# Kernel optimization log

Hardware: AMD Instinct MI355X
Metric: run time of the kernel (lower is better)

The kernel has to match this reference:

```python
import jax, jax.numpy as jnp
import numpy as np

D, H = 256, 4            # model dim, num heads
HD = D // H              # head dim (even, needed by rotate_half)
B, N, M, NS = 2, 6, 512, 512  # batch, views, t keypoints, s keypoints
EPS = 1e-5


def _linear(x, w, b):
    return x @ w + b


def _ln(x, g, b):
    mu = x.mean(-1, keepdims=True)
    var = ((x - mu) ** 2).mean(-1, keepdims=True)
    return (x - mu) * jax.lax.rsqrt(var + EPS) * g + b


def _ffn(x, f1w, f1b, lng, lnb, f2w, f2b):
    # Linear(2d,2d) -> LayerNorm -> exact GELU -> Linear(2d,d)
    h = jax.nn.gelu(_ln(_linear(x, f1w, f1b), lng, lnb), approximate=False)
    return _linear(h, f2w, f2b)


def _rotate_half(x):
    # pairs (x0,x1) -> (-x1, x0), interleaved
    return jnp.stack((-x[..., 1::2], x[..., 0::2]), axis=-1).reshape(x.shape)


def _rope(freqs, t):
    return t * freqs[0] + _rotate_half(t) * freqs[1]


def _attn(q, k, v):
    sim = jnp.einsum('...id,...jd->...ij', q, k) * (q.shape[-1] ** -0.5)
    return jnp.einsum('...ij,...jd->...id', jax.nn.softmax(sim, axis=-1), v)


def _self_block(x, enc, qkv_w, qkv_b, out_w, out_b, *ffn_p):
    b, n_img, m, d = x.shape
    enc = jnp.swapaxes(enc, 2, 3)  # encoding.dim()==6 path
    qkv = _linear(x, qkv_w, qkv_b).reshape(b, n_img, m, H, HD, 3)
    qkv = jnp.swapaxes(qkv, -4, -3)  # [b,N,H,m,hd,3]
    q, k, v = qkv[..., 0], qkv[..., 1], qkv[..., 2]
    ctx = _attn(_rope(enc, q), _rope(enc, k), v)  # [b,N,H,m,hd]
    msg = _linear(jnp.swapaxes(ctx, -3, -2).reshape(b, n_img, m, d), out_w, out_b)
    return x + _ffn(jnp.concatenate([x, msg], -1), *ffn_p)


def _t2t_block(t, qkv_w, qkv_b, out_w, out_b, *ffn_p):
    t2 = jnp.swapaxes(t, 1, 2)  # [b,m,N,d]
    b, m, n_img, d = t2.shape
    qkv = _linear(t2, qkv_w, qkv_b).reshape(b, m, n_img, H, HD, 3)
    qkv = jnp.swapaxes(qkv, 3, 2)  # [b,m,H,N,hd,3]
    q, k, v = qkv[..., 0], qkv[..., 1], qkv[..., 2]
    ctx = _attn(q, k, v)  # [b,m,H,N,hd]
    msg = _linear(jnp.swapaxes(ctx, 3, 2).reshape(b, m, n_img, d), out_w, out_b)
    return jnp.swapaxes(t2 + _ffn(jnp.concatenate([t2, msg], -1), *ffn_p), 1, 2)


def _s2s_block(s, q_enc, k_enc, qkv_w, qkv_b, out_w, out_b, *ffn_p):
    b, n_img, n, d = s.shape
    qkv = _linear(s, qkv_w, qkv_b).reshape(b, n_img, n, H, HD, 3)
    qkv = jnp.swapaxes(jnp.swapaxes(qkv, -4, -3), -5, -4)  # [b,H,N,n,hd,3]
    q, k, v = qkv[..., 0], qkv[..., 1], qkv[..., 2]
    # expand queries across all views, RoPE per (i,j) view pair
    q = jnp.broadcast_to(q[:, :, None], (b, H, n_img, n_img, n, HD))
    q = _rope(q_enc, q).reshape(b, H, n_img, n_img * n, HD)
    k = _rope(k_enc, k)
    ctx = _attn(q, k, v).reshape(b, H, n_img, n_img, n, HD)
    # drop diagonal (i==j) entries exactly like boolean-mask indexing in torch
    off = np.nonzero(~np.eye(n_img, dtype=bool).ravel())[0]
    ctx = ctx.reshape(b, H, n_img * n_img, n, HD)[:, :, off]
    ctx = ctx.reshape(b, H, n_img - 1, n_img, n, HD).mean(2)  # [b,H,N,n,hd]
    ctx = jnp.swapaxes(jnp.swapaxes(ctx, 1, 2), 2, 3).reshape(b, n_img, n, d)
    msg = _linear(ctx, out_w, out_b)
    return s + _ffn(jnp.concatenate([s, msg], -1), *ffn_p)


def _cross_block(d0, d1, q_w, q_b, kv_w, kv_b, out_w, out_b, *ffn_p):
    b, n_img, m, d = d0.shape
    m1 = d1.shape[2]
    q = jnp.swapaxes(_linear(d0, q_w, q_b).reshape(b, n_img, m, H, HD), 2, 3)
    kv = jnp.swapaxes(_linear(d1, kv_w, kv_b).reshape(b, n_img, m1, H, HD, 2), 2, 3)
    ctx = _attn(q, kv[..., 0], kv[..., 1])  # [b,N,H,m,hd]
    msg = _linear(jnp.swapaxes(ctx, 2, 3).reshape(b, n_img, m, d), out_w, out_b)
    return d0 + _ffn(jnp.concatenate([d0, msg], -1), *ffn_p)


def setup_inputs() -> dict:
    key = jax.random.key(0)
    ks = iter(jax.random.split(key, 80))
    f32 = jnp.float32

    def lin(din, dout):
        return (jax.random.normal(next(ks), (din, dout), f32) * (din ** -0.5),
                jnp.zeros((dout,), f32))

    inp = {}
    inp['t_desc'] = jax.random.normal(next(ks), (B, N, M, D), f32)
    inp['s_desc'] = jax.random.normal(next(ks), (B, N, NS, D), f32)
    inp['t_encoding'] = jax.random.normal(next(ks), (2, 1, 1, N, M, HD), f32)
    inp['s_encoding'] = jax.random.normal(next(ks), (2, 1, 1, N, NS, HD), f32)
    inp['q_encoding'] = jax.random.normal(next(ks), (2, 1, 1, N, N, 1, HD), f32)
    inp['k_encoding'] = jax.random.normal(next(ks), (2, 1, 1, N, NS, HD), f32)
    for pre in ('sa', 'ss', 'tt'):
        inp[pre + '_qkv_w'], inp[pre + '_qkv_b'] = lin(D, 3 * D)
        inp[pre + '_out_w'], inp[pre + '_out_b'] = lin(D, D)
        inp[pre + '_f1_w'], inp[pre + '_f1_b'] = lin(2 * D, 2 * D)
        inp[pre + '_ln_g'] = jnp.ones((2 * D,), f32)
        inp[pre + '_ln_b'] = jnp.zeros((2 * D,), f32)
        inp[pre + '_f2_w'], inp[pre + '_f2_b'] = lin(2 * D, D)
    inp['ca_q_w'], inp['ca_q_b'] = lin(D, D)
    inp['ca_kv_w'], inp['ca_kv_b'] = lin(D, 2 * D)
    inp['ca_out_w'], inp['ca_out_b'] = lin(D, D)
    inp['ca_f1_w'], inp['ca_f1_b'] = lin(2 * D, 2 * D)
    inp['ca_ln_g'] = jnp.ones((2 * D,), f32)
    inp['ca_ln_b'] = jnp.zeros((2 * D,), f32)
    inp['ca_f2_w'], inp['ca_f2_b'] = lin(2 * D, D)
    inp['cf_w1'], inp['cf_b1'] = lin(D, D)
    inp['cf_w2'], inp['cf_b2'] = lin(D, 1)
    return inp


def reference(t_desc, s_desc, t_encoding, s_encoding, q_encoding, k_encoding,
              sa_qkv_w, sa_qkv_b, sa_out_w, sa_out_b, sa_f1_w, sa_f1_b, sa_ln_g, sa_ln_b, sa_f2_w, sa_f2_b,
              ss_qkv_w, ss_qkv_b, ss_out_w, ss_out_b, ss_f1_w, ss_f1_b, ss_ln_g, ss_ln_b, ss_f2_w, ss_f2_b,
              tt_qkv_w, tt_qkv_b, tt_out_w, tt_out_b, tt_f1_w, tt_f1_b, tt_ln_g, tt_ln_b, tt_f2_w, tt_f2_b,
              ca_q_w, ca_q_b, ca_kv_w, ca_kv_b, ca_out_w, ca_out_b, ca_f1_w, ca_f1_b, ca_ln_g, ca_ln_b, ca_f2_w, ca_f2_b,
              cf_w1, cf_b1, cf_w2, cf_b2):
    sa = (sa_qkv_w, sa_qkv_b, sa_out_w, sa_out_b, sa_f1_w, sa_f1_b, sa_ln_g, sa_ln_b, sa_f2_w, sa_f2_b)
    t = _self_block(t_desc, t_encoding, *sa)   # shared SelfBlock weights
    s = _self_block(s_desc, s_encoding, *sa)
    t = _t2t_block(t, tt_qkv_w, tt_qkv_b, tt_out_w, tt_out_b, tt_f1_w, tt_f1_b, tt_ln_g, tt_ln_b, tt_f2_w, tt_f2_b)
    s = _s2s_block(s, q_encoding, k_encoding, ss_qkv_w, ss_qkv_b, ss_out_w, ss_out_b, ss_f1_w, ss_f1_b, ss_ln_g, ss_ln_b, ss_f2_w, ss_f2_b)
    ca = (ca_q_w, ca_q_b, ca_kv_w, ca_kv_b, ca_out_w, ca_out_b, ca_f1_w, ca_f1_b, ca_ln_g, ca_ln_b, ca_f2_w, ca_f2_b)
    t2 = _cross_block(t, s, *ca)               # shared CrossBlock weights
    s2 = _cross_block(s, t, *ca)
    conf = _linear(jax.nn.relu(_linear(jax.lax.stop_gradient(s), cf_w1, cf_b1)), cf_w2, cf_b2)[..., 0]
    return t2, s2, conf
```

## Files before the change

### kernel.cpp

```cpp
#include <hip/hip_runtime.h>
#include <hip/hip_bf16.h>
#include <math.h>

constexpr int kD   = 256;
constexpr int kH   = 4;
constexpr int kHD  = 64;
constexpr int kB   = 2;
constexpr int kN   = 6;
constexpr int kM   = 512;
constexpr int kRowsH = kB*kN*kM;
constexpr int kRows  = 2*kRowsH;
constexpr int kGrpH  = kB*kN*kH;
constexpr int kGrp   = 2*kGrpH;
constexpr size_t kTOK = (size_t)kRowsH*kD;
constexpr size_t kEncSlab = (size_t)kN*kM*kHD;
constexpr size_t kQEncSlab = (size_t)kN*kN*kHD;
constexpr float kL2E = 1.4426950408889634f;

typedef unsigned short u16;
typedef __attribute__((ext_vector_type(8))) short s16x8;
typedef __attribute__((ext_vector_type(4))) float f32x4;

__device__ __forceinline__ float wred_sum(float v){
  #pragma unroll
  for (int m=32;m>0;m>>=1) v += __shfl_xor(v, m, 64);
  return v;
}
__device__ __forceinline__ u16 f2b(float x){
  union { float f; unsigned u; } a; a.f = x;
  unsigned r = a.u + 0x7fffu + ((a.u >> 16) & 1u);
  return (u16)(r >> 16);
}
__device__ __forceinline__ float b2f(u16 x){
  union { unsigned u; float f; } a; a.u = ((unsigned)x) << 16;
  return a.f;
}
__device__ __forceinline__ unsigned pk2(float lo, float hi){
  union { __hip_bfloat162 h2; unsigned u; } c;
  c.h2 = __float22bfloat162_rn(make_float2(lo, hi));
  return c.u;
}

struct FuseArgs {
  const float* Wout[4]; const float* W1[4];
  const float* bout[4]; const float* b1[4];
  float* Wtmp; float* b1p;
};

__global__ __launch_bounds__(256) void wfuse_k(FuseArgs fa)
{
  const int set = blockIdx.x >> 5;
  const int t = blockIdx.x & 31;
  const int row0 = (t >> 3)*64, col0 = (t & 7)*64;
  const float* A  = fa.Wout[set];
  const float* Bm = fa.W1[set] + 256*512;
  float* C = fa.Wtmp + (size_t)set*(256*512);
  __shared__ float As[16][65];
  __shared__ float Bs[16][64];
  const int tid = threadIdx.x;
  const int tx = tid & 15, ty = tid >> 4;
  const int ar = tid >> 2, ak = (tid & 3)*4;
  const int wr = tid >> 4, wc = (tid & 15)*4;
  float acc[4][4] = {};
  for (int kt = 0; kt < 256; kt += 16) {
    float4 av = *(const float4*)(A + (size_t)(row0+ar)*256 + kt + ak);
    As[ak+0][ar]=av.x; As[ak+1][ar]=av.y; As[ak+2][ar]=av.z; As[ak+3][ar]=av.w;
    *(float4*)(&Bs[wr][wc]) = *(const float4*)(Bm + (size_t)(kt+wr)*512 + col0 + wc);
    __syncthreads();
    #pragma unroll
    for (int k2=0;k2<16;++k2) {
      float a[4], b[4];
      #pragma unroll
      for (int i=0;i<4;++i) a[i]=As[k2][ty*4+i];
      #pragma unroll
      for (int j=0;j<4;++j) b[j]=Bs[k2][tx*4+j];
      #pragma unroll
      for (int i=0;i<4;++i)
        #pragma unroll
        for (int j=0;j<4;++j) acc[i][j] = fmaf(a[i], b[j], acc[i][j]);
    }
    __syncthreads();
  }
  #pragma unroll
  for (int i=0;i<4;++i)
    #pragma unroll
    for (int j=0;j<4;++j)
      C[(size_t)(row0+ty*4+i)*512 + col0+tx*4+j] = acc[i][j];
}

__global__ __launch_bounds__(256) void biasfuse_k(FuseArgs fa)
{
  const int set = blockIdx.x >> 1;
  const int n = (blockIdx.x & 1)*256 + threadIdx.x;
  const float* W1 = fa.W1[set];
  const float* bo = fa.bout[set];
  float s = fa.b1[set][n];
  for (int k = 0; k < 256; ++k)
    s = fmaf(bo[k], W1[(size_t)(256+k)*512 + n], s);
  fa.b1p[set*512 + n] = s;
}

struct WtDesc { const float* W; const float* W2; u16* Wt; int K; int N; int ntiles; };
struct WtTable { WtDesc d[18]; };

__global__ __launch_bounds__(256) void wtcast_k(WtTable tab)
{
  int t = blockIdx.x, mi = 0;
  while (t >= tab.d[mi].ntiles) { t -= tab.d[mi].ntiles; ++mi; }
  const float* W = tab.d[mi].W;
  const float* W2 = tab.d[mi].W2;
  u16* Wt = tab.d[mi].Wt;
  const int K = tab.d[mi].K, N = tab.d[mi].N;
  const int ktn = K >> 5;
  const int nt = t / ktn, kt = t % ktn;
  const int n0 = nt*128, k0 = kt*32;
  u16* dst = Wt + (size_t)t*4096;
  #pragma unroll
  for (int s = 0; s < 2; ++s) {
    const int idx0 = (s*256 + (int)threadIdx.x)*8;
    const int ar = idx0 >> 5;
    const int w8 = (idx0 >> 3) & 3;
    const int sw = (ar >> 1) & 3;
    int kk = k0 + ((w8 ^ sw) << 3);
    const int n  = n0 + ar;
    const float* src = W;
    if (W2 && kk >= 256) { src = W2; kk -= 256; }
    union { u16 u[8]; s16x8 v; } o;
    #pragma unroll
    for (int e = 0; e < 8; ++e)
      o.u[e] = f2b(src[(size_t)(kk + e)*N + n]);
    *(s16x8*)(dst + idx0) = o.v;
  }
}

template<bool A1B, bool A2B, bool CB>
__global__ __launch_bounds__(256) void mmad_k(
    const void* __restrict__ A1a, const void* __restrict__ A1b,
    const void* __restrict__ A2a, const void* __restrict__ A2b, int K1,
    const u16* __restrict__ Wa, const u16* __restrict__ Wb,
    const float* __restrict__ bia, const float* __restrict__ bib,
    const float* __restrict__ bi2a, const float* __restrict__ bi2b, int Ns,
    const float* __restrict__ Ra, const float* __restrict__ Rb,
    void* __restrict__ Cp, int N, int K, int Mh, int doRelu)
{
  __shared__ u16 As[2][128*32];
  __shared__ u16 Bs[2][128*32];
  const int tid = threadIdx.x;
  const int lane = tid & 63, w = tid >> 6;
  const int gx = gridDim.x;
  const int nblk = gx * gridDim.y;
  int flat = blockIdx.y*gx + blockIdx.x;
  if (!(nblk & 7)) flat = (flat & 7)*(nblk >> 3) + (flat >> 3);
  const int bxx = flat % gx, byy = flat / gx;
  const int row0 = byy*128, col0 = bxx*128;
  const bool sec = (row0 >= Mh);
  const int lr0 = sec ? row0 - Mh : row0;
  const void* A1 = sec ? A1b : A1a;
  const void* A2 = sec ? A2b : A2a;
  const u16* Wt  = sec ? Wb : Wa;
  const float* bias  = sec ? bib : bia;
  const float* bias2 = sec ? bi2b : bi2a;
  const float* R = sec ? Rb : Ra;
  const int wr = (w >> 1)*64, wc = (w & 1)*64;
  const int ar = tid >> 1, ah = tid & 1;
  const int K2 = K - K1;
  const int ktn = K >> 5;
  f32x4 acc[4][4] = {};

  auto stage = [&](int buf, int kt) {
    const u16* wtile = Wt + ((size_t)((col0 >> 7)*ktn + (kt >> 5)))*4096;
    #pragma unroll
    for (int s = 0; s < 2; ++s) {
      const u16* srcp = wtile + (size_t)(s*256 + tid)*8;
      __builtin_amdgcn_global_load_lds(
          (const __attribute__((address_space(1))) void*)srcp,
          (__attribute__((address_space(3))) void*)((char*)Bs[buf] + s*4096 + w*1024),
          16, 0, 0);
    }
    const int kk = kt + ah*16;
    union { u16 u[16]; s16x8 v[2]; } tmp;
    if (kk < K1) {
      if constexpr (A1B) {
        const u16* ap = (const u16*)A1 + (size_t)(lr0+ar)*K1 + kk;
        tmp.v[0] = *(const s16x8*)ap; tmp.v[1] = *(const s16x8*)(ap+8);
      } else {
        const float* ap = (const float*)A1 + (size_t)(lr0+ar)*K1 + kk;
        #pragma unroll
        for (int i = 0; i < 16; i += 4) {
          f32x4 v4 = *(const f32x4*)(ap + i);
          tmp.u[i+0]=f2b(v4.x); tmp.u[i+1]=f2b(v4.y); tmp.u[i+2]=f2b(v4.z); tmp.u[i+3]=f2b(v4.w);
        }
      }
    } else {
      if constexpr (A2B) {
        const u16* ap = (const u16*)A2 + (size_t)(lr0+ar)*K2 + (kk - K1);
        tmp.v[0] = *(const s16x8*)ap; tmp.v[1] = *(const s16x8*)(ap+8);
      } else {
        const float* ap = (const float*)A2 + (size_t)(lr0+ar)*K2 + (kk - K1);
        #pragma unroll
        for (int i = 0; i < 16; i += 4) {
          f32x4 v4 = *(const f32x4*)(ap + i);
          tmp.u[i+0]=f2b(v4.x); tmp.u[i+1]=f2b(v4.y); tmp.u[i+2]=f2b(v4.z); tmp.u[i+3]=f2b(v4.w);
        }
      }
    }
    const int sw = (ar >> 1) & 3;
    *(s16x8*)(&As[buf][ar*32 + ((ah*2+0)^sw)*8]) = tmp.v[0];
    *(s16x8*)(&As[buf][ar*32 + ((ah*2+1)^sw)*8]) = tmp.v[1];
  };

  stage(0, 0);
  __syncthreads();
  for (int t = 0; t < ktn; ++t) {
    const int cur = t & 1;
    if (t + 1 < ktn) stage(cur ^ 1, (t + 1) << 5);
    s16x8 af[4], bfv[4];
    #pragma unroll
    for (int fm = 0; fm < 4; ++fm) {
      const int r = wr + fm*16 + (lane & 15);
      const int g = (lane >> 4) ^ ((r >> 1) & 3);
      af[fm] = *(const s16x8*)(&As[cur][r*32 + g*8]);
    }
    #pragma unroll
    for (int fn = 0; fn < 4; ++fn) {
      const int c = wc + fn*16 + (lane & 15);
      const int g = (lane >> 4) ^ ((c >> 1) & 3);
      bfv[fn] = *(const s16x8*)(&Bs[cur][c*32 + g*8]);
    }
    #pragma unroll
    for (int fm = 0; fm < 4; ++fm)
      #pragma unroll
      for (int fn = 0; fn < 4; ++fn)
        acc[fm][fn] = __builtin_amdgcn_mfma_f32_16x16x32_bf16(af[fm], bfv[fn], acc[fm][fn], 0, 0, 0);
    __syncthreads();
  }

  #pragma unroll
  for (int fm = 0; fm < 4; ++fm) {
    const int ro = wr + fm*16 + (lane >> 4)*4;
    #pragma unroll
    for (int fn = 0; fn < 4; ++fn) {
      const int cc = col0 + wc + fn*16 + (lane & 15);
      const float bv = (cc < Ns) ? bias[cc] : bias2[cc - Ns];
      #pragma unroll
      for (int j = 0; j < 4; ++j) {
        float v = acc[fm][fn][j] + bv;
        if (R) v += R[(size_t)(lr0 + ro + j)*N + cc];
        if (doRelu) v = fmaxf(v, 0.f);
        const size_t idx = (size_t)(row0 + ro + j)*N + cc;
        if constexpr (CB) ((u16*)Cp)[idx] = f2b(v);
        else              ((float*)Cp)[idx] = v;
      }
    }
  }
}

__global__ __launch_bounds__(256) void prep_self_k(
    const u16* __restrict__ qkvU, const float* __restrict__ t_enc,
    const float* __restrict__ s_enc,
    u16* __restrict__ Qb, u16* __restrict__ Kb, u16* __restrict__ Vt)
{
  __shared__ u16 vs[64][66];
  const int g = blockIdx.x >> 3, i0 = (blockIdx.x & 7)*64;
  const int h = g & 3, bn = g >> 2;
  const float* enc = (bn < 12) ? t_enc : s_enc;
  const int n = (bn < 12 ? bn : bn - 12) % kN;
  const int c = threadIdx.x & 63, t4 = threadIdx.x >> 6;
  const float sgn = (c & 1) ? 1.f : -1.f;
  #pragma unroll 4
  for (int rr = 0; rr < 16; ++rr) {
    const int il = rr*4 + t4, i = i0 + il;
    const u16* base = qkvU + ((size_t)bn*kM + i)*768 + h*192;
    const float q = b2f(base[c*3]), k = b2f(base[c*3+1]);
    const float qp = b2f(base[(c^1)*3]), kp = b2f(base[(c^1)*3+1]);
    const size_t eo = ((size_t)(n*kM + i))*kHD + c;
    const float e0 = enc[eo], e1 = enc[kEncSlab + eo];
    Qb[((size_t)g*kM + i)*kHD + c] = f2b((q*e0 + sgn*qp*e1)*0.125f);
    Kb[((size_t)g*kM + i)*kHD + c] = f2b(k*e0 + sgn*kp*e1);
    vs[il][c] = base[c*3+2];
  }
  __syncthreads();
  #pragma unroll 4
  for (int rr = 0; rr < 16; ++rr) {
    const int cc = rr*4 + t4;
    Vt[((size_t)g*kHD + cc)*kM + i0 + c] = vs[c][cc];
  }
}

__global__ __launch_bounds__(256) void prep_s2s_k(
    const u16* __restrict__ qkvU, const float* __restrict__ kenc,
    float* __restrict__ Qs, u16* __restrict__ Kb, u16* __restrict__ Vt)
{
  __shared__ u16 vs[64][66];
  const int g = blockIdx.x >> 3, i0 = (blockIdx.x & 7)*64;
  const int view = g % kN, bh = g / kN;
  const int h = bh & 3, b = bh >> 2;
  const int c = threadIdx.x & 63, t4 = threadIdx.x >> 6;
  const float sgn = (c & 1) ? 1.f : -1.f;
  #pragma unroll 4
  for (int rr = 0; rr < 16; ++rr) {
    const int il = rr*4 + t4, i = i0 + il;
    const u16* base = qkvU + ((size_t)(kRowsH + (b*kN+view)*kM + i))*768 + h*192;
    const float k = b2f(base[c*3+1]), kp = b2f(base[(c^1)*3+1]);
    const size_t eo = ((size_t)(view*kM + i))*kHD + c;
    const float e0 = kenc[eo], e1 = kenc[kEncSlab + eo];
    Qs[((size_t)g*kM + i)*kHD + c] = b2f(base[c*3]);
    Kb[((size_t)g*kM + i)*kHD + c] = f2b(k*e0 + sgn*kp*e1);
    vs[il][c] = base[c*3+2];
  }
  __syncthreads();
  #pragma unroll 4
  for (int rr = 0; rr < 16; ++rr) {
    const int cc = rr*4 + t4;
    Vt[((size_t)g*kHD + cc)*kM + i0 + c] = vs[c][cc];
  }
}

__global__ __launch_bounds__(256) void prep_cross_k(
    const u16* __restrict__ qkvC, u16* __restrict__ Kb, u16* __restrict__ Vt)
{
  __shared__ u16 vs[64][66];
  const int g = blockIdx.x >> 3, i0 = (blockIdx.x & 7)*64;
  const int h = g & 3, bn = g >> 2;
  const int src = (bn < 12) ? bn + 12 : bn - 12;
  const int c = threadIdx.x & 63, t4 = threadIdx.x >> 6;
  #pragma unroll 4
  for (int rr = 0; rr < 16; ++rr) {
    const int il = rr*4 + t4, i = i0 + il;
    const u16* base = qkvC + ((size_t)src*kM + i)*768 + 256 + h*128;
    Kb[((size_t)g*kM + i)*kHD + c] = f2b(b2f(base[c*2]) * 0.125f);
    vs[il][c] = base[c*2+1];
  }
  __syncthreads();
  #pragma unroll 4
  for (int rr = 0; rr < 16; ++rr) {
    const int cc = rr*4 + t4;
    Vt[((size_t)g*kHD + cc)*kM + i0 + c] = vs[c][cc];
  }
}

template<int CROSSQ>
__global__ __launch_bounds__(256) void attn_mm_k(
    const u16* __restrict__ Qb, const u16* __restrict__ Kb,
    const u16* __restrict__ Vt, u16* __restrict__ ctx)
{
  const int w = threadIdx.x >> 6, lane = threadIdx.x & 63;
  const int bij = (blockIdx.x & 7)*48 + (blockIdx.x >> 3);
  const int g = bij >> 2, qblk = bij & 3;
  const int h = g & 3, bn = g >> 2;
  const int q0 = qblk*128 + w*32;
  const int qr = lane & 15, hi = lane >> 4;
  const bool subhi = (hi & 1), up = (hi >= 2);

  s16x8 qf0[2], qf1[2];
  #pragma unroll
  for (int f = 0; f < 2; ++f) {
    const u16* qp = CROSSQ
      ? Qb + ((size_t)(bn*kM + q0 + f*16 + qr))*768 + h*kHD + hi*8
      : Qb + ((size_t)g*kM + q0 + f*16 + qr)*kHD + hi*8;
    qf0[f] = *(const s16x8*)(qp);
    qf1[f] = *(const s16x8*)(qp + 32);
  }

  const u16* Kg = Kb + (size_t)g*kM*kHD;
  const u16* Vg = Vt + (size_t)g*kHD*kM;
  f32x4 acc[2][4] = {};
  float m[2] = {-1e30f, -1e30f}, l[2] = {0.f, 0.f};

  for (int kc = 0; kc < 16; ++kc) {
    const int k0 = kc*32;
    s16x8 a0[2], a1[2];
    #pragma unroll
    for (int t = 0; t < 2; ++t) {
      const u16* kp = Kg + ((size_t)(k0 + t*16 + qr))*kHD + hi*8;
      a0[t] = *(const s16x8*)(kp);
      a1[t] = *(const s16x8*)(kp + 32);
    }
    s16x8 pa[2];
    #pragma unroll
    for (int f = 0; f < 2; ++f) {
      f32x4 st[2];
      #pragma unroll
      for (int t = 0; t < 2; ++t) {
        f32x4 z = {0.f, 0.f, 0.f, 0.f};
        z = __builtin_amdgcn_mfma_f32_16x16x32_bf16(a0[t], qf0[f], z, 0, 0, 0);
        z = __builtin_amdgcn_mfma_f32_16x16x32_bf16(a1[t], qf1[f], z, 0, 0, 0);
        st[t] = z;
      }
      float mloc = fmaxf(fmaxf(fmaxf(st[0][0], st[0][1]), fmaxf(st[0][2], st[0][3])),
                         fmaxf(fmaxf(st[1][0], st[1][1]), fmaxf(st[1][2], st[1][3])));
      mloc = fmaxf(mloc, __shfl_xor(mloc, 16));
      mloc = fmaxf(mloc, __shfl_xor(mloc, 32));
      if (!__all(mloc - m[f] <= 8.f)) {
        const float mn = fmaxf(m[f], mloc);
        const float r = exp2f((m[f] - mn)*kL2E);
        m[f] = mn;
        l[f] *= r;
        const float rr0 = __shfl(r, hi*4+0), rr1 = __shfl(r, hi*4+1);
        const float rr2 = __shfl(r, hi*4+2), rr3 = __shfl(r, hi*4+3);
        #pragma unroll
        for (int db = 0; db < 4; ++db) {
          acc[f][db][0] *= rr0; acc[f][db][1] *= rr1;
          acc[f][db][2] *= rr2; acc[f][db][3] *= rr3;
        }
      }
      float p[8], ls = 0.f;
      #pragma unroll
      for (int t = 0; t < 2; ++t)
        #pragma unroll
        for (int j = 0; j < 4; ++j) {
          const float pv = exp2f((st[t][j] - m[f])*kL2E);
          p[t*4+j] = pv; ls += pv;
        }
      l[f] += ls;
      const unsigned c00 = pk2(p[0], p[1]);
      const unsigned c01 = pk2(p[2], p[3]);
      const unsigned c10 = pk2(p[4], p[5]);
      const unsigned c11 = pk2(p[6], p[7]);
      const unsigned c00x = __shfl_xor((int)c00, 32), c10x = __shfl_xor((int)c10, 32);
      const unsigned c01x = __shfl_xor((int)c01, 32), c11x = __shfl_xor((int)c11, 32);
      const unsigned E = up ? c10x : c00, F = up ? c10 : c00x;
      const unsigned G = up ? c11x : c01, H = up ? c11 : c01x;
      const unsigned Ex = __shfl_xor((int)E, 16), Fx = __shfl_xor((int)F, 16);
      const unsigned Gx = __shfl_xor((int)G, 16), Hx = __shfl_xor((int)H, 16);
      union { unsigned w[4]; s16x8 v; } pw;
      pw.w[0] = subhi ? Fx : E;
      pw.w[1] = subhi ? Hx : G;
      pw.w[2] = subhi ? F  : Ex;
      pw.w[3] = subhi ? H  : Gx;
      pa[f] = pw.v;
    }
    #pragma unroll
    for (int db = 0; db < 4; ++db) {
      const u16* vp = Vg + ((size_t)(db*16 + qr))*kM + k0 + hi*8;
      const s16x8 vf = *(const s16x8*)(vp);
      acc[0][db] = __builtin_amdgcn_mfma_f32_16x16x32_bf16(pa[0], vf, acc[0][db], 0, 0, 0);
      acc[1][db] = __builtin_amdgcn_mfma_f32_16x16x32_bf16(pa[1], vf, acc[1][db], 0, 0, 0);
    }
  }

  #pragma unroll
  for (int f = 0; f < 2; ++f) {
    float lf = l[f];
    lf += __shfl_xor(lf, 16); lf += __shfl_xor(lf, 32);
    const float li = 1.f/lf;
    const float l0 = __shfl(li, hi*4+0), l1 = __shfl(li, hi*4+1);
    const float l2 = __shfl(li, hi*4+2), l3 = __shfl(li, hi*4+3);
    #pragma unroll
    for (int db = 0; db < 4; ++db) {
      const size_t base = ((size_t)(bn*kM + q0 + f*16 + hi*4))*kD + h*kHD + db*16 + qr;
      ctx[base + 0*kD] = f2b(acc[f][db][0]*l0);
      ctx[base + 1*kD] = f2b(acc[f][db][1]*l1);
      ctx[base + 2*kD] = f2b(acc[f][db][2]*l2);
      ctx[base + 3*kD] = f2b(acc[f][db][3]*l3);
    }
  }
}

__device__ __forceinline__ void rope4(const f32x4 x, const f32x4 e0, const f32x4 e1, float o[4])
{
  o[0] = x[0]*e0[0] - x[1]*e1[0];
  o[1] = x[1]*e0[1] + x[0]*e1[1];
  o[2] = x[2]*e0[2] - x[3]*e1[2];
  o[3] = x[3]*e0[3] + x[2]*e1[3];
}

__global__ __launch_bounds__(256) void attn_s2s_k(
    const float* __restrict__ Qraw, const u16* __restrict__ Kb,
    const u16* __restrict__ Vt, const float* __restrict__ qenc,
    u16* __restrict__ ctx5)
{
  const int w = threadIdx.x >> 6, lane = threadIdx.x & 63;
  const int bij = (blockIdx.x & 7)*120 + (blockIdx.x >> 3);
  const int bh = bij / 120;
  const int rest = bij % 120;
  const int col = rest / 20;
  const int rem = rest % 20;
  const int qblk = rem / 5, split = rem % 5;
  const int q0 = qblk*128 + w*32;
  const int qr = lane & 15, hi = lane >> 4;
  const bool subhi = (hi & 1), up = (hi >= 2);

  const int e  = split*6 + col;
  const int iv = e/5;
  const int j0 = e%5;
  const int jv = j0 + (j0 >= iv ? 1 : 0);

  s16x8 qf0[2], qf1[2];
  #pragma unroll
  for (int f = 0; f < 2; ++f) {
    const float* qp = Qraw + ((size_t)(bh*kN + jv)*kM + q0 + f*16 + qr)*kHD + hi*8;
    const float* ep = qenc + ((size_t)(iv*kN + jv))*kHD + hi*8;
    union { u16 u[8]; s16x8 v; } A, B;
    float o[4];
    rope4(*(const f32x4*)(qp),   *(const f32x4*)(ep),   *(const f32x4*)(ep+kQEncSlab), o);
    #pragma unroll
    for (int j = 0; j < 4; ++j) A.u[j] = f2b(o[j]*0.125f);
    rope4(*(const f32x4*)(qp+4), *(const f32x4*)(ep+4), *(const f32x4*)(ep+kQEncSlab+4), o);
    #pragma unroll
    for (int j = 0; j < 4; ++j) A.u[4+j] = f2b(o[j]*0.125f);
    rope4(*(const f32x4*)(qp+32), *(const f32x4*)(ep+32), *(const f32x4*)(ep+kQEncSlab+32), o);
    #pragma unroll
    for (int j = 0; j < 4; ++j) B.u[j] = f2b(o[j]*0.125f);
    rope4(*(const f32x4*)(qp+36), *(const f32x4*)(ep+36), *(const f32x4*)(ep+kQEncSlab+36), o);
    #pragma unroll
    for (int j = 0; j < 4; ++j) B.u[4+j] = f2b(o[j]*0.125f);
    qf0[f] = A.v; qf1[f] = B.v;
  }

  const int g2 = bh*kN + iv;
  const u16* Kg = Kb + (size_t)g2*kM*kHD;
  const u16* Vg = Vt + (size_t)g2*kHD*kM;
  f32x4 acc[2][4] = {};
  float m[2] = {-1e30f, -1e30f}, l[2] = {0.f, 0.f};

  for (int kc = 0; kc < 16; ++kc) {
    const int k0 = kc*32;
    s16x8 a0[2], a1[2];
    #pragma unroll
    for (int t = 0; t < 2; ++t) {
      const u16* kp = Kg + ((size_t)(k0 + t*16 + qr))*kHD + hi*8;
      a0[t] = *(const s16x8*)(kp);
      a1[t] = *(const s16x8*)(kp + 32);
    }
    s16x8 pa[2];
    #pragma unroll
    for (int f = 0; f < 2; ++f) {
      f32x4 st[2];
      #pragma unroll
      for (int t = 0; t < 2; ++t) {
        f32x4 z = {0.f, 0.f, 0.f, 0.f};
        z = __builtin_amdgcn_mfma_f32_16x16x32_bf16(a0[t], qf0[f], z, 0, 0, 0);
        z = __builtin_amdgcn_mfma_f32_16x16x32_bf16(a1[t], qf1[f], z, 0, 0, 0);
        st[t] = z;
      }
      float mloc = fmaxf(fmaxf(fmaxf(st[0][0], st[0][1]), fmaxf(st[0][2], st[0][3])),
                         fmaxf(fmaxf(st[1][0], st[1][1]), fmaxf(st[1][2], st[1][3])));
      mloc = fmaxf(mloc, __shfl_xor(mloc, 16));
      mloc = fmaxf(mloc, __shfl_xor(mloc, 32));
      if (!__all(mloc - m[f] <= 8.f)) {
        const float mn = fmaxf(m[f], mloc);
        const float r = exp2f((m[f] - mn)*kL2E);
        m[f] = mn;
        l[f] *= r;
        const float rr0 = __shfl(r, hi*4+0), rr1 = __shfl(r, hi*4+1);
        const float rr2 = __shfl(r, hi*4+2), rr3 = __shfl(r, hi*4+3);
        #pragma unroll
        for (int db = 0; db < 4; ++db) {
          acc[f][db][0] *= rr0; acc[f][db][1] *= rr1;
          acc[f][db][2] *= rr2; acc[f][db][3] *= rr3;
        }
      }
      float p[8], ls = 0.f;
      #pragma unroll
      for (int t = 0; t < 2; ++t)
        #pragma unroll
        for (int j = 0; j < 4; ++j) {
          const float pv = exp2f((st[t][j] - m[f])*kL2E);
          p[t*4+j] = pv; ls += pv;
        }
      l[f] += ls;
      const unsigned c00 = pk2(p[0], p[1]);
      const unsigned c01 = pk2(p[2], p[3]);
      const unsigned c10 = pk2(p[4], p[5]);
      const unsigned c11 = pk2(p[6], p[7]);
      const unsigned c00x = __shfl_xor((int)c00, 32), c10x = __shfl_xor((int)c10, 32);
      const unsigned c01x = __shfl_xor((int)c01, 32), c11x = __shfl_xor((int)c11, 32);
      const unsigned E = up ? c10x : c00, F = up ? c10 : c00x;
      const unsigned G = up ? c11x : c01, H = up ? c11 : c01x;
      const unsigned Ex = __shfl_xor((int)E, 16), Fx = __shfl_xor((int)F, 16);
      const unsigned Gx = __shfl_xor((int)G, 16), Hx = __shfl_xor((int)H, 16);
      union { unsigned w[4]; s16x8 v; } pw;
      pw.w[0] = subhi ? Fx : E;
      pw.w[1] = subhi ? Hx : G;
      pw.w[2] = subhi ? F  : Ex;
      pw.w[3] = subhi ? H  : Gx;
      pa[f] = pw.v;
    }
    #pragma unroll
    for (int db = 0; db < 4; ++db) {
      const u16* vp = Vg + ((size_t)(db*16 + qr))*kM + k0 + hi*8;
      const s16x8 vf = *(const s16x8*)(vp);
      acc[0][db] = __builtin_amdgcn_mfma_f32_16x16x32_bf16(pa[0], vf, acc[0][db], 0, 0, 0);
      acc[1][db] = __builtin_amdgcn_mfma_f32_16x16x32_bf16(pa[1], vf, acc[1][db], 0, 0, 0);
    }
  }

  const int b = bh >> 2, h = bh & 3;
  u16* outp = ctx5 + (size_t)split*kTOK;
  #pragma unroll
  for (int f = 0; f < 2; ++f) {
    float lf = l[f];
    lf += __shfl_xor(lf, 16); lf += __shfl_xor(lf, 32);
    const float li = 0.2f/lf;
    const float l0 = __shfl(li, hi*4+0), l1 = __shfl(li, hi*4+1);
    const float l2 = __shfl(li, hi*4+2), l3 = __shfl(li, hi*4+3);
    #pragma unroll
    for (int db = 0; db < 4; ++db) {
      const size_t base = ((size_t)((b*kN + col)*kM + q0 + f*16 + hi*4))*kD + h*kHD + db*16 + qr;
      outp[base + 0*kD] = f2b(acc[f][db][0]*l0);
      outp[base + 1*kD] = f2b(acc[f][db][1]*l1);
      outp[base + 2*kD] = f2b(acc[f][db][2]*l2);
      outp[base + 3*kD] = f2b(acc[f][db][3]*l3);
    }
  }
}

__global__ __launch_bounds__(256) void sum5_k(const u16* __restrict__ c5,
                                              u16* __restrict__ outU)
{
  const size_t i4 = ((size_t)blockIdx.x*256 + threadIdx.x)*4;
  float s0=0.f, s1=0.f, s2=0.f, s3=0.f;
  #pragma unroll
  for (int sp = 0; sp < 5; ++sp) {
    uint2 d = *(const uint2*)(c5 + sp*kTOK + i4);
    s0 += b2f((u16)(d.x & 0xffff)); s1 += b2f((u16)(d.x >> 16));
    s2 += b2f((u16)(d.y & 0xffff)); s3 += b2f((u16)(d.y >> 16));
  }
  union { u16 u[4]; uint2 d; } o;
  o.u[0]=f2b(s0); o.u[1]=f2b(s1); o.u[2]=f2b(s2); o.u[3]=f2b(s3);
  *(uint2*)(outU + i4) = o.d;
}

__global__ __launch_bounds__(256) void attn_t2t_k(
    const u16* __restrict__ qkvU, u16* __restrict__ ctxU)
{
  const int wid = blockIdx.x*4 + (threadIdx.x >> 6);
  const int lane = threadIdx.x & 63;
  const int m = wid & 511;
  const int t = wid >> 9;
  const int nq = t % kN;
  const int bh = t / kN;
  const int h = bh & 3, b = bh >> 2;
  const u16* pb[kN];
  #pragma unroll
  for (int nk = 0; nk < kN; ++nk)
    pb[nk] = qkvU + ((size_t)(b*kN+nk)*kM + m)*768 + h*192;
  const float qc = b2f(pb[nq][lane*3]);
  float sim[kN];
  #pragma unroll
  for (int nk = 0; nk < kN; ++nk)
    sim[nk] = wred_sum(qc * b2f(pb[nk][lane*3+1])) * 0.125f;
  float mx = sim[0];
  #pragma unroll
  for (int nk = 1; nk < kN; ++nk) mx = fmaxf(mx, sim[nk]);
  float p[kN], s = 0.f;
  #pragma unroll
  for (int nk = 0; nk < kN; ++nk) { p[nk] = expf(sim[nk]-mx); s += p[nk]; }
  const float inv = 1.f/s;
  float o = 0.f;
  #pragma unroll
  for (int nk = 0; nk < kN; ++nk) o = fmaf(p[nk], b2f(pb[nk][lane*3+2]), o);
  ctxU[((size_t)(b*kN+nq)*kM + m)*kD + h*kHD + lane] = f2b(o*inv);
}

__global__ __launch_bounds__(256) void lngelu_k(
    const float* __restrict__ x, u16* __restrict__ y,
    const float* __restrict__ g0, const float* __restrict__ b0,
    const float* __restrict__ g1, const float* __restrict__ b1, int Mh)
{
  const int row = blockIdx.x;
  const int tid = threadIdx.x;
  const float* g = (row < Mh) ? g0 : g1;
  const float* bb = (row < Mh) ? b0 : b1;
  const float* xr = x + (size_t)row*512;
  const float v0 = xr[tid], v1 = xr[tid+256];
  const int w = tid >> 6, lane = tid & 63;
  __shared__ float red[2][4];
  const float s1 = wred_sum(v0+v1);
  const float s2 = wred_sum(v0*v0+v1*v1);
  if (lane == 0){ red[0][w]=s1; red[1][w]=s2; }
  __syncthreads();
  const float mean = (red[0][0]+red[0][1]+red[0][2]+red[0][3]) * (1.f/512.f);
  const float ms   = (red[1][0]+red[1][1]+red[1][2]+red[1][3]) * (1.f/512.f);
  const float rs = rsqrtf(ms - mean*mean + 1e-5f);
  const float y0 = (v0-mean)*rs*g[tid]     + bb[tid];
  const float y1 = (v1-mean)*rs*g[tid+256] + bb[tid+256];
  y[(size_t)row*512 + tid]     = f2b(0.5f*y0*(1.f+erff(y0*0.70710678118654752f)));
  y[(size_t)row*512 + tid+256] = f2b(0.5f*y1*(1.f+erff(y1*0.70710678118654752f)));
}

__global__ void conf_dot_k(const float* __restrict__ tmp, const float* __restrict__ w2,
                           const float* __restrict__ b2, float* __restrict__ out)
{
  const int w = threadIdx.x >> 6, lane = threadIdx.x & 63;
  const int row = blockIdx.x*4 + w;
  const float* t = tmp + (size_t)row*kD;
  float s = 0.f;
  #pragma unroll
  for (int j=0;j<4;++j) s = fmaf(t[lane+j*64], w2[lane+j*64], s);
  s = wred_sum(s);
  if (lane == 0) out[row] = s + b2[0];
}

extern "C" void kernel_launch(void* const* d_in, const int* in_sizes, int n_in,
                              void* d_out, int out_size, void* d_ws, size_t ws_size,
                              hipStream_t stream)
{
  auto F = [&](int i){ return (const float*)d_in[i]; };
  const float* t_desc = F(0);
  const float* s_desc = F(1);
  const float* t_enc  = F(2);
  const float* s_enc  = F(3);
  const float* q_enc  = F(4);
  const float* k_enc  = F(5);

  char* base = (char*)d_ws;
  float* xts = (float*)base;
  float* xt = xts;
  float* xs = xts + kTOK;
  char* R1  = base + 2*kTOK*sizeof(float);
  char* CTX = R1 + 4*kTOK*sizeof(float);
  char* MSG = CTX + 2*kTOK*sizeof(u16);
  u16* Qb16 = (u16*)(MSG + kTOK*sizeof(float));
  u16* Kb16 = Qb16 + 2*kTOK;
  u16* Vt16 = Kb16 + 2*kTOK;
  u16* wsW  = Vt16 + 2*kTOK;
  u16*   qkvU  = (u16*)R1;
  float* hbuf  = (float*)R1;
  u16*   ctx5  = (u16*)R1;
  float* Wtmp  = (float*)R1;
  u16*   ctxU  = (u16*)CTX;
  float* Qs2s  = (float*)MSG;
  float* confb = (float*)MSG;
  u16*   yU    = (u16*)CTX;

  float* out_t2s2 = (float*)d_out;
  float* out_conf = (float*)d_out + 2*kTOK;

  WtTable tab;
  int nd = 0, total_tiles = 0;
  size_t woff = 0;
  const u16* wp[18];
  auto addw = [&](int idx, const float* W2, int K, int N){
    u16* dst = wsW + woff;
    tab.d[nd] = { F(idx), W2, dst, K, N, (N>>7)*(K>>5) };
    total_tiles += tab.d[nd].ntiles;
    wp[nd] = dst;
    woff += (size_t)K*N;
    ++nd;
    return nd-1;
  };
  const int W_SA_QKV = addw(6,  nullptr, 256, 768);
  const int W_SA_F1  = addw(10, Wtmp + 0*131072, 512, 512);
  const int W_SA_F2  = addw(14, nullptr, 512, 256);
  const int W_SS_QKV = addw(16, nullptr, 256, 768);
  const int W_SS_F1  = addw(20, Wtmp + 1*131072, 512, 512);
  const int W_SS_F2  = addw(24, nullptr, 512, 256);
  const int W_TT_QKV = addw(26, nullptr, 256, 768);
  const int W_TT_F1  = addw(30, Wtmp + 2*131072, 512, 512);
  const int W_TT_F2  = addw(34, nullptr, 512, 256);
  const int W_CA_Q   = addw(36, nullptr, 256, 256);
  const int W_CA_KV  = addw(38, nullptr, 256, 512);
  const int W_CA_F1  = addw(42, Wtmp + 3*131072, 512, 512);
  const int W_CA_F2  = addw(46, nullptr, 512, 256);
  const int W_CF_1   = addw(48, nullptr, 256, 256);
  (void)W_CA_KV;
  float* b1p = (float*)(wsW + woff);

  FuseArgs fa;
  fa.Wout[0]=F(8);  fa.Wout[1]=F(18); fa.Wout[2]=F(28); fa.Wout[3]=F(40);
  fa.W1[0]=F(10);   fa.W1[1]=F(20);   fa.W1[2]=F(30);   fa.W1[3]=F(42);
  fa.bout[0]=F(9);  fa.bout[1]=F(19); fa.bout[2]=F(29); fa.bout[3]=F(41);
  fa.b1[0]=F(11);   fa.b1[1]=F(21);   fa.b1[2]=F(31);   fa.b1[3]=F(43);
  fa.Wtmp = Wtmp; fa.b1p = b1p;
  wfuse_k<<<128, 256, 0, stream>>>(fa);
  biasfuse_k<<<8, 256, 0, stream>>>(fa);
  wtcast_k<<<total_tiles, 256, 0, stream>>>(tab);

  auto mm_f32_to_b16 = [&](const float* a1a, const float* a1b, int wa, int wb2,
                           const float* ba, const float* bb2, u16* c, int N_, int K_){
    dim3 grid(N_/128, kRows/128);
    mmad_k<false,false,true><<<grid,256,0,stream>>>(a1a, a1b, nullptr, nullptr, K_,
        wp[wa], wp[wb2], ba, bb2, ba, bb2, N_, nullptr, nullptr, c, N_, K_, kRowsH, 0);
  };
  auto mm_f1 = [&](const float* a1a, const float* a1b, const u16* a2a, const u16* a2b,
                   int wa, int wb2, const float* ba, const float* bb2, float* c){
    dim3 grid(512/128, kRows/128);
    mmad_k<false,true,false><<<grid,256,0,stream>>>(a1a, a1b, a2a, a2b, 256,
        wp[wa], wp[wb2], ba, bb2, ba, bb2, 512, nullptr, nullptr, c, 512, 512, kRowsH, 0);
  };
  auto mm_f2 = [&](const u16* a1a, const u16* a1b, int wa, int wb2,
                   const float* ba, const float* bb2,
                   const float* ra, const float* rb, float* c){
    dim3 grid(256/128, kRows/128);
    mmad_k<true,false,false><<<grid,256,0,stream>>>(a1a, a1b, nullptr, nullptr, 512,
        wp[wa], wp[wb2], ba, bb2, ba, bb2, 256, ra, rb, c, 256, 512, kRowsH, 0);
  };

  mm_f32_to_b16(t_desc, s_desc, W_SA_QKV, W_SA_QKV, F(7), F(7), qkvU, 768, 256);
  prep_self_k<<<kGrp*8, 256, 0, stream>>>(qkvU, t_enc, s_enc, Qb16, Kb16, Vt16);
  attn_mm_k<0><<<384, 256, 0, stream>>>(Qb16, Kb16, Vt16, ctxU);
  mm_f1(t_desc, s_desc, ctxU, ctxU + kTOK, W_SA_F1, W_SA_F1, b1p+0*512, b1p+0*512, hbuf);
  lngelu_k<<<kRows, 256, 0, stream>>>(hbuf, yU, F(12), F(13), F(12), F(13), kRowsH);
  mm_f2(yU, yU + (size_t)kRowsH*512, W_SA_F2, W_SA_F2, F(15), F(15), t_desc, s_desc, xts);

  mm_f32_to_b16(xt, xs, W_TT_QKV, W_SS_QKV, F(27), F(17), qkvU, 768, 256);
  prep_s2s_k<<<kGrpH*8, 256, 0, stream>>>(qkvU, k_enc, Qs2s, Kb16, Vt16);
  attn_t2t_k<<<(kB*kH*kN*kM)/4, 256, 0, stream>>>(qkvU, ctxU);
  attn_s2s_k<<<960, 256, 0, stream>>>(Qs2s, Kb16, Vt16, q_enc, ctx5);
  sum5_k<<<(int)(kTOK/1024), 256, 0, stream>>>(ctx5, ctxU + kTOK);
  mm_f1(xt, xs, ctxU, ctxU + kTOK, W_TT_F1, W_SS_F1, b1p+2*512, b1p+1*512, hbuf);
  lngelu_k<<<kRows, 256, 0, stream>>>(hbuf, yU, F(32), F(33), F(22), F(23), kRowsH);
  mm_f2(yU, yU + (size_t)kRowsH*512, W_TT_F2, W_SS_F2, F(35), F(25), xt, xs, xts);

  {
    dim3 grid(2, kRowsH/128);
    mmad_k<false,false,false><<<grid,256,0,stream>>>(xs, xs, nullptr, nullptr, 256,
        wp[W_CF_1], wp[W_CF_1], F(49), F(49), F(49), F(49), 256,
        nullptr, nullptr, confb, 256, 256, kRowsH, 1);
  }
  conf_dot_k<<<kRowsH/4, 256, 0, stream>>>(confb, F(50), F(51), out_conf);

  {
    dim3 grid(768/128, kRows/128);
    mmad_k<false,false,true><<<grid,256,0,stream>>>(xt, xs, nullptr, nullptr, 256,
        wp[W_CA_Q], wp[W_CA_Q], F(37), F(37), F(39), F(39), 256,
        nullptr, nullptr, qkvU, 768, 256, kRowsH, 0);
  }
  prep_cross_k<<<kGrp*8, 256, 0, stream>>>(qkvU, Kb16, Vt16);
  attn_mm_k<1><<<384, 256, 0, stream>>>(qkvU, Kb16, Vt16, ctxU);
  mm_f1(xt, xs, ctxU, ctxU + kTOK, W_CA_F1, W_CA_F1, b1p+3*512, b1p+3*512, hbuf);
  lngelu_k<<<kRows, 256, 0, stream>>>(hbuf, yU, F(44), F(45), F(44), F(45), kRowsH);
  mm_f2(yU, yU + (size_t)kRowsH*512, W_CA_F2, W_CA_F2, F(47), F(47), xt, xs, out_t2s2);
}
```

Baseline: 480.5 us.

## Software-pipeline QK^T and softmax/PV stages in flash attention loops

```diff
diff --git a/kernel.cpp b/kernel.cpp
--- a/kernel.cpp
+++ b/kernel.cpp
@@ -367,28 +367,35 @@
   f32x4 acc[2][4] = {};
   float m[2] = {-1e30f, -1e30f}, l[2] = {0.f, 0.f};
 
-  for (int kc = 0; kc < 16; ++kc) {
-    const int k0 = kc*32;
-    s16x8 a0[2], a1[2];
+  s16x8 kA[2][2], kB[2][2];
+  f32x4 sA[2][2], sB[2][2];
+
+  auto loadK = [&](s16x8 kb[2][2], int kc){
     #pragma unroll
     for (int t = 0; t < 2; ++t) {
-      const u16* kp = Kg + ((size_t)(k0 + t*16 + qr))*kHD + hi*8;
-      a0[t] = *(const s16x8*)(kp);
-      a1[t] = *(const s16x8*)(kp + 32);
-    }
-    s16x8 pa[2];
-    #pragma unroll
-    for (int f = 0; f < 2; ++f) {
-      f32x4 st[2];
+      const u16* kp = Kg + ((size_t)(kc*32 + t*16 + qr))*kHD + hi*8;
+      kb[t][0] = *(const s16x8*)(kp);
+      kb[t][1] = *(const s16x8*)(kp + 32);
+    }
+  };
+  auto qk = [&](const s16x8 kb[2][2], f32x4 st[2][2]){
+    #pragma unroll
+    for (int f = 0; f < 2; ++f)
       #pragma unroll
       for (int t = 0; t < 2; ++t) {
         f32x4 z = {0.f, 0.f, 0.f, 0.f};
-        z = __builtin_amdgcn_mfma_f32_16x16x32_bf16(a0[t], qf0[f], z, 0, 0, 0);
-        z = __builtin_amdgcn_mfma_f32_16x16x32_bf16(a1[t], qf1[f], z, 0, 0, 0);
-        st[t] = z;
+        z = __builtin_amdgcn_mfma_f32_16x16x32_bf16(kb[t][0], qf0[f], z, 0, 0, 0);
+        z = __builtin_amdgcn_mfma_f32_16x16x32_bf16(kb[t][1], qf1[f], z, 0, 0, 0);
+        st[f][t] = z;
       }
-      float mloc = fmaxf(fmaxf(fmaxf(st[0][0], st[0][1]), fmaxf(st[0][2], st[0][3])),
-                         fmaxf(fmaxf(st[1][0], st[1][1]), fmaxf(st[1][2], st[1][3])));
+  };
+  auto smpv = [&](f32x4 st[2][2], int kc){
+    const int k0 = kc*32;
+    s16x8 pa[2];
+    #pragma unroll
+    for (int f = 0; f < 2; ++f) {
+      float mloc = fmaxf(fmaxf(fmaxf(st[f][0][0], st[f][0][1]), fmaxf(st[f][0][2], st[f][0][3])),
+                         fmaxf(fmaxf(st[f][1][0], st[f][1][1]), fmaxf(st[f][1][2], st[f][1][3])));
       mloc = fmaxf(mloc, __shfl_xor(mloc, 16));
       mloc = fmaxf(mloc, __shfl_xor(mloc, 32));
       if (!__all(mloc - m[f] <= 8.f)) {
@@ -409,7 +416,7 @@
       for (int t = 0; t < 2; ++t)
         #pragma unroll
         for (int j = 0; j < 4; ++j) {
-          const float pv = exp2f((st[t][j] - m[f])*kL2E);
+          const float pv = exp2f((st[f][t][j] - m[f])*kL2E);
           p[t*4+j] = pv; ls += pv;
         }
       l[f] += ls;
@@ -432,11 +439,22 @@
     }
     #pragma unroll
     for (int db = 0; db < 4; ++db) {
-      const u16* vp = Vg + ((size_t)(db*16 + qr))*kM + k0 + hi*8;
-      const s16x8 vf = *(const s16x8*)(vp);
+      const s16x8 vf = *(const s16x8*)(Vg + ((size_t)(db*16 + qr))*kM + k0 + hi*8);
       acc[0][db] = __builtin_amdgcn_mfma_f32_16x16x32_bf16(pa[0], vf, acc[0][db], 0, 0, 0);
       acc[1][db] = __builtin_amdgcn_mfma_f32_16x16x32_bf16(pa[1], vf, acc[1][db], 0, 0, 0);
     }
+  };
+
+  loadK(kA, 0);
+  qk(kA, sA);
+  loadK(kB, 1);
+  for (int kc = 0; kc < 16; kc += 2) {
+    qk(kB, sB);
+    if (kc + 2 < 16) loadK(kA, kc + 2);
+    smpv(sA, kc);
+    if (kc + 2 < 16) qk(kA, sA);
+    if (kc + 3 < 16) loadK(kB, kc + 3);
+    smpv(sB, kc + 1);
   }
 
   #pragma unroll
@@ -514,28 +532,35 @@
   f32x4 acc[2][4] = {};
   float m[2] = {-1e30f, -1e30f}, l[2] = {0.f, 0.f};
 
-  for (int kc = 0; kc < 16; ++kc) {
-    const int k0 = kc*32;
-    s16x8 a0[2], a1[2];
+  s16x8 kA[2][2], kB[2][2];
+  f32x4 sA[2][2], sB[2][2];
+
+  auto loadK = [&](s16x8 kb[2][2], int kc){
     #pragma unroll
     for (int t = 0; t < 2; ++t) {
-      const u16* kp = Kg + ((size_t)(k0 + t*16 + qr))*kHD + hi*8;
-      a0[t] = *(const s16x8*)(kp);
-      a1[t] = *(const s16x8*)(kp + 32);
-    }
-    s16x8 pa[2];
-    #pragma unroll
-    for (int f = 0; f < 2; ++f) {
-      f32x4 st[2];
+      const u16* kp = Kg + ((size_t)(kc*32 + t*16 + qr))*kHD + hi*8;
+      kb[t][0] = *(const s16x8*)(kp);
+      kb[t][1] = *(const s16x8*)(kp + 32);
+    }
+  };
+  auto qk = [&](const s16x8 kb[2][2], f32x4 st[2][2]){
+    #pragma unroll
+    for (int f = 0; f < 2; ++f)
       #pragma unroll
       for (int t = 0; t < 2; ++t) {
         f32x4 z = {0.f, 0.f, 0.f, 0.f};
-        z = __builtin_amdgcn_mfma_f32_16x16x32_bf16(a0[t], qf0[f], z, 0, 0, 0);
-        z = __builtin_amdgcn_mfma_f32_16x16x32_bf16(a1[t], qf1[f], z, 0, 0, 0);
-        st[t] = z;
+        z = __builtin_amdgcn_mfma_f32_16x16x32_bf16(kb[t][0], qf0[f], z, 0, 0, 0);
+        z = __builtin_amdgcn_mfma_f32_16x16x32_bf16(kb[t][1], qf1[f], z, 0, 0, 0);
+        st[f][t] = z;
       }
-      float mloc = fmaxf(fmaxf(fmaxf(st[0][0], st[0][1]), fmaxf(st[0][2], st[0][3])),
-                         fmaxf(fmaxf(st[1][0], st[1][1]), fmaxf(st[1][2], st[1][3])));
+  };
+  auto smpv = [&](f32x4 st[2][2], int kc){
+    const int k0 = kc*32;
+    s16x8 pa[2];
+    #pragma unroll
+    for (int f = 0; f < 2; ++f) {
+      float mloc = fmaxf(fmaxf(fmaxf(st[f][0][0], st[f][0][1]), fmaxf(st[f][0][2], st[f][0][3])),
+                         fmaxf(fmaxf(st[f][1][0], st[f][1][1]), fmaxf(st[f][1][2], st[f][1][3])));
       mloc = fmaxf(mloc, __shfl_xor(mloc, 16));
       mloc = fmaxf(mloc, __shfl_xor(mloc, 32));
       if (!__all(mloc - m[f] <= 8.f)) {
@@ -556,7 +581,7 @@
       for (int t = 0; t < 2; ++t)
         #pragma unroll
         for (int j = 0; j < 4; ++j) {
-          const float pv = exp2f((st[t][j] - m[f])*kL2E);
+          const float pv = exp2f((st[f][t][j] - m[f])*kL2E);
           p[t*4+j] = pv; ls += pv;
         }
       l[f] += ls;
@@ -579,11 +604,22 @@
     }
     #pragma unroll
     for (int db = 0; db < 4; ++db) {
-      const u16* vp = Vg + ((size_t)(db*16 + qr))*kM + k0 + hi*8;
-      const s16x8 vf = *(const s16x8*)(vp);
+      const s16x8 vf = *(const s16x8*)(Vg + ((size_t)(db*16 + qr))*kM + k0 + hi*8);
       acc[0][db] = __builtin_amdgcn_mfma_f32_16x16x32_bf16(pa[0], vf, acc[0][db], 0, 0, 0);
       acc[1][db] = __builtin_amdgcn_mfma_f32_16x16x32_bf16(pa[1], vf, acc[1][db], 0, 0, 0);
     }
+  };
+
+  loadK(kA, 0);
+  qk(kA, sA);
+  loadK(kB, 1);
+  for (int kc = 0; kc < 16; kc += 2) {
+    qk(kB, sB);
+    if (kc + 2 < 16) loadK(kA, kc + 2);
+    smpv(sA, kc);
+    if (kc + 2 < 16) qk(kA, sA);
+    if (kc + 3 < 16) loadK(kB, kc + 3);
+    smpv(sB, kc + 1);
   }
 
   const int b = bh >> 2, h = bh & 3;
```

Result: no change. 473.4 us (-1.5%).
